# Kernel optimization log

Hardware: AMD Instinct MI355X
Metric: run time of the kernel (lower is better)

## Reference

```python
import jax, jax.numpy as jnp
import numpy as np

N_WIRES = 16
VAR_DEPTH = 2
BATCH = 16


def _param_sizes():
    sizes = []
    n = N_WIRES
    lay = 0
    while n > 1:
        sizes.append(4 * int(np.ceil(N_WIRES / 2 ** lay)) * VAR_DEPTH)
        n = (n + 1) // 2
        lay += 1
    return sizes  # [128, 64, 32, 16]


def _apply_1q(psi, gate, w):
    # psi: (B, 2, ..., 2); gate: (2,2) complex; wire w lives on axis w+1
    psi = jnp.moveaxis(psi, w + 1, -1)
    psi = jnp.einsum('...j,ij->...i', psi, gate)
    return jnp.moveaxis(psi, -1, w + 1)


def _rx(psi, th, w):
    c = jnp.cos(th / 2).astype(jnp.complex64)
    s = jnp.sin(th / 2).astype(jnp.complex64)
    gate = jnp.stack([jnp.stack([c, -1j * s]), jnp.stack([-1j * s, c])])
    return _apply_1q(psi, gate, w)


def _rz(psi, th, w):
    ph = jnp.exp(0.5j * th * jnp.array([-1.0, 1.0], jnp.float32)).astype(jnp.complex64)
    shape = [1] * psi.ndim
    shape[w + 1] = 2
    return psi * ph.reshape(shape)


def _rzz(psi, th, wa, wb):
    # diag(e^{-i t/2}, e^{i t/2}, e^{i t/2}, e^{-i t/2}) -> sign = -1 if bits equal else +1
    sgn = jnp.array([[-1.0, 1.0], [1.0, -1.0]], jnp.float32)
    ph = jnp.exp(0.5j * th * sgn).astype(jnp.complex64)  # symmetric, transpose-safe
    a, b = min(wa, wb) + 1, max(wa, wb) + 1
    shape = [1] * psi.ndim
    shape[a] = 2
    shape[b] = 2
    return psi * ph.reshape(shape)


def _cnot(psi, c, t):
    p0 = jax.lax.slice_in_dim(psi, 0, 1, axis=c + 1)
    p1 = jax.lax.slice_in_dim(psi, 1, 2, axis=c + 1)
    return jnp.concatenate([p0, jnp.flip(p1, axis=t + 1)], axis=c + 1)


def _conv_layer(psi, params, active):
    n = len(active)
    for d in range(VAR_DEPTH):
        for j in range(n):
            base = 4 * j + d * 4 * n
            psi = _rx(psi, params[base + 0], active[j])
            psi = _rz(psi, params[base + 1], active[j])
            psi = _rx(psi, params[base + 2], active[j])
        for bg in (0, 1):
            for j in range(bg, n, 2):
                jn = (j + 1) % n  # ring coupling (wraps last->first)
                base = 4 * j + d * 4 * n
                psi = _rzz(psi, params[base + 3], active[j], active[jn])
    return psi


def _pool(psi, active):
    for j in range(0, len(active), 2):
        if j + 1 < len(active):
            psi = _cnot(psi, active[j], active[j + 1])
    return psi, active[::2]


def _forward(psi, params_list):
    active = list(range(N_WIRES))
    for p in params_list:
        psi = _conv_layer(psi, p, active)
        if len(active) > 1:
            psi, active = _pool(psi, active)
    w = active[0]  # measure Z on the surviving wire (wire 0)
    prob = psi.real ** 2 + psi.imag ** 2
    axes = tuple(a for a in range(1, psi.ndim) if a != w + 1)
    p2 = prob.sum(axis=axes)  # (B, 2)
    return p2[:, 0] - p2[:, 1]


def setup_inputs() -> dict:
    key = jax.random.key(0)
    ks = jax.random.split(key, 8)
    dim = 2 ** N_WIRES
    x_re = jax.random.normal(ks[0], (BATCH, dim), dtype=jnp.float32)
    x_im = jax.random.normal(ks[1], (BATCH, dim), dtype=jnp.float32)
    nrm = jnp.sqrt(jnp.sum(x_re ** 2 + x_im ** 2, axis=1, keepdims=True))
    x_re = x_re / nrm
    x_im = x_im / nrm
    sizes = _param_sizes()
    two_pi = 2.0 * np.pi
    params = [jax.random.uniform(ks[2 + i], (sizes[i],), dtype=jnp.float32) * two_pi
              for i in range(len(sizes))]
    return {"x_re": x_re, "x_im": x_im,
            "params0": params[0], "params1": params[1],
            "params2": params[2], "params3": params[3]}


def reference(x_re, x_im, params0, params1, params2, params3):
    psi = (x_re + 1j * x_im).astype(jnp.complex64)
    psi = psi.reshape((BATCH,) + (2,) * N_WIRES)
    return _forward(psi, [params0, params1, params2, params3])
```

## Files before the change

kernel.cpp:

```cpp
#include <hip/hip_runtime.h>


#define DEV __device__ __forceinline__
#define TB(i) (tbl + (i)*8)

__device__ static const unsigned char G_CP[60] = {
  15,14,13,12,11,10,9,8,7,6,5,4,3,2,1,0,
  15,14,13,12,11,10,9,8,7,6,5,4,3,2,1,0,
  15,13,11,9,7,5,3,1,
  15,13,11,9,7,5,3,1,
  15,11,7,3,
  15,11,7,3,
  15,7,
  15,7
};
__device__ static const unsigned char G_CQ[60] = {
  14,13,12,11,10,9,8,7,6,5,4,3,2,1,0,15,
  14,13,12,11,10,9,8,7,6,5,4,3,2,1,0,15,
  13,11,9,7,5,3,1,15,
  13,11,9,7,5,3,1,15,
  11,7,3,15,
  11,7,3,15,
  7,15,
  7,15
};

DEV float2 F2(float x, float y){ float2 r; r.x = x; r.y = y; return r; }
DEV float2 cmulf(float2 a, float2 b){ return F2(a.x*b.x - a.y*b.y, a.x*b.y + a.y*b.x); }
DEV int swz(int j){ return j ^ ((j>>4)&15) ^ ((j>>6)&15); }

template<int B>
DEV void gate8(float2* a, const float* __restrict__ g){
  float u00r=g[0],u00i=g[1],u01r=g[2],u01i=g[3],u10r=g[4],u10i=g[5],u11r=g[6],u11i=g[7];
  #pragma unroll
  for (int m=0; m<4; m++){
    int i0 = ((m>>B)<<(B+1)) | (m & ((1<<B)-1));
    int i1 = i0 | (1<<B);
    float2 x0=a[i0], x1=a[i1];
    a[i0] = F2(u00r*x0.x - u00i*x0.y + u01r*x1.x - u01i*x1.y,
               u00r*x0.y + u00i*x0.x + u01r*x1.y + u01i*x1.x);
    a[i1] = F2(u10r*x0.x - u10i*x0.y + u11r*x1.x - u11i*x1.y,
               u10r*x0.y + u10i*x0.x + u11r*x1.y + u11i*x1.x);
  }
}

template<int CB,int TB>
DEV void cnot8(float2* a){
  #pragma unroll
  for (int r=0; r<8; r++){
    if ( ((r>>CB)&1)==1 && ((r>>TB)&1)==0 ){
      float2 tmp = a[r]; a[r] = a[r | (1<<TB)]; a[r | (1<<TB)] = tmp;
    }
  }
}

template<int C0,int N,unsigned M0,unsigned M1,unsigned M2>
DEV void diag8(float2* a, const float* __restrict__ tbl, unsigned Ib){
  const unsigned regmask = M0|M1|M2;
  float2 F0 = F2(1.f, 0.f);
  #pragma unroll
  for (int k=0; k<N; k++){
    const int p = G_CP[C0+k], q = G_CQ[C0+k];
    if ( !(((1u<<p)|(1u<<q)) & regmask) ){
      float c = tbl[480 + 2*(C0+k)], s = tbl[481 + 2*(C0+k)];
      unsigned x = ((Ib>>p) ^ (Ib>>q)) & 1u;
      F0 = cmulf(F0, F2(c, x ? s : -s));
    }
  }
  #pragma unroll
  for (int r=0; r<8; r++){
    unsigned Ir = Ib ^ ((r&1)?M0:0u) ^ ((r&2)?M1:0u) ^ ((r&4)?M2:0u);
    float2 ph = F0;
    #pragma unroll
    for (int k=0; k<N; k++){
      const int p = G_CP[C0+k], q = G_CQ[C0+k];
      if ( ((1u<<p)|(1u<<q)) & regmask ){
        float c = tbl[480 + 2*(C0+k)], s = tbl[481 + 2*(C0+k)];
        unsigned x = ((Ir>>p) ^ (Ir>>q)) & 1u;
        ph = cmulf(ph, F2(c, x ? s : -s));
      }
    }
    a[r] = cmulf(a[r], ph);
  }
}

__global__ void k_setup(const float* __restrict__ p0, const float* __restrict__ p1,
                        const float* __restrict__ p2, const float* __restrict__ p3,
                        float* __restrict__ tbl, float* __restrict__ out){
  int g = threadIdx.x;
  if (g < 16) out[g] = 0.f;
  if (g >= 60) return;
  int d, j, n; const float* P;
  if (g < 32)      { n=16; d=(g>>4)&1; j=g&15; P=p0; }
  else if (g < 48) { n=8;  d=(g>>3)&1; j=g&7;  P=p1; }
  else if (g < 56) { n=4;  d=(g>>2)&1; j=g&3;  P=p2; }
  else             { n=2;  d=(g>>1)&1; j=g&1;  P=p3; }
  int base = 4*j + 4*n*d;
  double th0 = P[base+0], th1 = P[base+1], th2 = P[base+2], th3 = P[base+3];
  double c0 = cos(th0*0.5), s0 = sin(th0*0.5);
  double ca = cos(th1*0.5), sa = sin(th1*0.5);
  double c2 = cos(th2*0.5), s2 = sin(th2*0.5);
  double B00r =  ca*c0, B00i = -sa*c0;
  double B01r = -sa*s0, B01i = -ca*s0;
  double B10r =  sa*s0, B10i = -ca*s0;
  double B11r =  ca*c0, B11i =  sa*c0;
  double U00r = c2*B00r + s2*B10i, U00i = c2*B00i - s2*B10r;
  double U01r = c2*B01r + s2*B11i, U01i = c2*B01i - s2*B11r;
  double U10r = s2*B00i + c2*B10r, U10i = -s2*B00r + c2*B10i;
  double U11r = s2*B01i + c2*B11r, U11i = -s2*B01r + c2*B11i;
  float* o = tbl + g*8;
  o[0]=(float)U00r; o[1]=(float)U00i; o[2]=(float)U01r; o[3]=(float)U01i;
  o[4]=(float)U10r; o[5]=(float)U10i; o[6]=(float)U11r; o[7]=(float)U11i;
  tbl[480 + 2*g] = (float)cos(th3*0.5);
  tbl[481 + 2*g] = (float)sin(th3*0.5);
}

__global__ __launch_bounds__(128) void k_pass1(const float* __restrict__ xre, const float* __restrict__ xim,
                                               const float* __restrict__ tbl, float2* __restrict__ st){
  const int t = threadIdx.x;
  const int batch = blockIdx.x >> 6, o = blockIdx.x & 63;
  const unsigned hi = ((unsigned)batch<<16) | ((unsigned)o<<10);
  __shared__ float2 lds[2][1024];
  float2 a[8];
  {
    unsigned base = hi | ((unsigned)t<<3);
    float4 r0 = *(const float4*)(xre+base), r1 = *(const float4*)(xre+base+4);
    float4 i0 = *(const float4*)(xim+base), i1 = *(const float4*)(xim+base+4);
    a[0]=F2(r0.x,i0.x); a[1]=F2(r0.y,i0.y); a[2]=F2(r0.z,i0.z); a[3]=F2(r0.w,i0.w);
    a[4]=F2(r1.x,i1.x); a[5]=F2(r1.y,i1.y); a[6]=F2(r1.z,i1.z); a[7]=F2(r1.w,i1.w);
  }
  gate8<0>(a, TB(15)); gate8<1>(a, TB(14)); gate8<2>(a, TB(13));
  #pragma unroll
  for (int r=0;r<8;r++) lds[0][swz(r | (t<<3))] = a[r];
  __syncthreads();
  #pragma unroll
  for (int r=0;r<8;r++) a[r] = lds[0][swz((t&7) | (r<<3) | ((t>>3)<<6))];
  gate8<0>(a, TB(12)); gate8<1>(a, TB(11)); gate8<2>(a, TB(10));
  #pragma unroll
  for (int r=0;r<8;r++) lds[1][swz((t&7) | (r<<3) | ((t>>3)<<6))] = a[r];
  __syncthreads();
  #pragma unroll
  for (int r=0;r<8;r++) a[r] = lds[1][swz((t&63) | (r<<6) | ((t>>6)<<9))];
  gate8<0>(a, TB(9)); gate8<1>(a, TB(8)); gate8<2>(a, TB(7));
  #pragma unroll
  for (int r=0;r<8;r++) lds[0][swz((t&63) | (r<<6) | ((t>>6)<<9))] = a[r];
  __syncthreads();
  #pragma unroll
  for (int r=0;r<8;r++) a[r] = lds[0][swz(t | (r<<7))];
  gate8<2>(a, TB(6));
  #pragma unroll
  for (int r=0;r<8;r++) st[hi | (unsigned)(t | (r<<7))] = a[r];
}

DEV unsigned p2I(int j, int o){ return (unsigned)((j&15) | (o<<4) | ((j>>4)<<10)); }

__global__ __launch_bounds__(128) void k_pass2(const float* __restrict__ tbl, float2* __restrict__ st){
  const int t = threadIdx.x;
  const int batch = blockIdx.x >> 6, o = blockIdx.x & 63;
  const unsigned bb = (unsigned)batch<<16;
  __shared__ float2 lds[2][1024];
  float2 a[8];
  #pragma unroll
  for (int r=0;r<8;r++) a[r] = st[bb | p2I(t | (r<<7), o)];
  gate8<0>(a, TB(2)); gate8<1>(a, TB(1)); gate8<2>(a, TB(0));
  #pragma unroll
  for (int r=0;r<8;r++) lds[0][swz(t | (r<<7))] = a[r];
  __syncthreads();
  #pragma unroll
  for (int r=0;r<8;r++) a[r] = lds[0][swz((t&15) | (r<<4) | ((t>>4)<<7))];
  gate8<0>(a, TB(5)); gate8<1>(a, TB(4)); gate8<2>(a, TB(3));
  diag8<0,16, (1u<<10),(1u<<11),(1u<<12)>(a, tbl, p2I((t&15) | ((t>>4)<<7), o));
  gate8<0>(a, TB(21)); gate8<1>(a, TB(20)); gate8<2>(a, TB(19));
  #pragma unroll
  for (int r=0;r<8;r++) lds[1][swz((t&15) | (r<<4) | ((t>>4)<<7))] = a[r];
  __syncthreads();
  #pragma unroll
  for (int r=0;r<8;r++) a[r] = lds[1][swz(t | (r<<7))];
  gate8<0>(a, TB(18)); gate8<1>(a, TB(17)); gate8<2>(a, TB(16));
  #pragma unroll
  for (int r=0;r<8;r++) lds[0][swz(t | (r<<7))] = a[r];
  __syncthreads();
  #pragma unroll
  for (int r=0;r<8;r++) a[r] = lds[0][swz(r | (t<<3))];
  gate8<0>(a, TB(31)); gate8<1>(a, TB(30)); gate8<2>(a, TB(29));
  #pragma unroll
  for (int r=0;r<8;r++) lds[1][swz(r | (t<<3))] = a[r];
  __syncthreads();
  #pragma unroll
  for (int r=0;r<8;r++) a[r] = lds[1][swz((t&7) | (r<<3) | ((t>>3)<<6))];
  gate8<0>(a, TB(28));
  #pragma unroll
  for (int r=0;r<8;r++) st[bb | p2I((t&7) | (r<<3) | ((t>>3)<<6), o)] = a[r];
}

__global__ __launch_bounds__(128) void k_pass3(const float* __restrict__ tbl, float2* __restrict__ st){
  const int t = threadIdx.x;
  const int batch = blockIdx.x >> 6, o = blockIdx.x & 63;
  const unsigned hi = ((unsigned)batch<<16) | ((unsigned)o<<10);
  __shared__ float2 lds[2][1024];
  float2 a[8];
  #pragma unroll
  for (int r=0;r<8;r++) a[r] = st[hi | (unsigned)((t&15) | (r<<4) | ((t>>4)<<7))];
  gate8<0>(a, TB(27)); gate8<1>(a, TB(26)); gate8<2>(a, TB(25));
  #pragma unroll
  for (int r=0;r<8;r++) lds[0][swz((t&15) | (r<<4) | ((t>>4)<<7))] = a[r];
  __syncthreads();
  #pragma unroll
  for (int r=0;r<8;r++) a[r] = lds[0][swz(t | (r<<7))];
  gate8<0>(a, TB(24)); gate8<1>(a, TB(23)); gate8<2>(a, TB(22));
  diag8<16,16, (1u<<7),(1u<<8),(1u<<9)>(a, tbl, (unsigned)t | ((unsigned)o<<10));
  #pragma unroll
  for (int r=0;r<8;r++) st[hi | (unsigned)(t | (r<<7))] = a[r];
}

DEV unsigned p4I(int j, unsigned og){
  return (unsigned)( (j&15) | (((j>>4)&1)<<5) | (((j>>5)&1)<<7) | (((j>>6)&1)<<9)
                   | (((j>>7)&1)<<11) | (((j>>8)&1)<<13) | (((j>>9)&1)<<15) ) | og;
}
DEV int p4_jA(int t,int r){ return t | (r<<7); }
DEV int p4_jB(int t,int r){ return (t&15) | (r<<4) | ((t>>4)<<7); }
DEV int p4_jC(int t,int r){ return (t&1) | ((r&1)<<1) | (((t>>1)&1)<<2) | (((r>>1)&1)<<3)
                                  | (((t>>2)&1)<<4) | (((r>>2)&1)<<5) | ((t>>3)<<6); }
DEV int p4_jD(int t,int r){ return (t&15) | ((r&1)<<4) | (((t>>4)&1)<<5) | (((r>>1)&1)<<6)
                                  | (((t>>5)&1)<<7) | (((r>>2)&1)<<8) | ((t>>6)<<9); }
DEV int p4_jF(int t,int r){ return (t&63) | ((r&1)<<6) | (((r>>1)&1)<<7) | (((t>>6)&1)<<8) | ((r>>2)<<9); }
DEV int p4_jG(int t,int r){ return (t&15) | ((r&3)<<4) | (((t>>4)&7)<<6) | ((r>>2)<<9); }
DEV int p4_jJ(int t,int r){ return (t&7) | ((r&1)<<3) | (((t>>3)&1)<<4) | (((r>>1)&1)<<5)
                                  | (((t>>4)&7)<<6) | ((r>>2)<<9); }

__global__ __launch_bounds__(128) void k_pass4(const float* __restrict__ tbl, float2* __restrict__ st,
                                               float* __restrict__ out){
  const int t = threadIdx.x;
  const int batch = blockIdx.x >> 6, o = blockIdx.x & 63;
  const unsigned bb = (unsigned)batch<<16;
  const unsigned og = ((unsigned)(o&1)<<4) | ((unsigned)(o&2)<<5) | ((unsigned)(o&4)<<6)
                    | ((unsigned)(o&8)<<7) | ((unsigned)(o&16)<<8) | ((unsigned)(o&32)<<9);
  __shared__ float2 lds[2][1024];
  float2 a[8];
  #pragma unroll
  for (int r=0;r<8;r++){
    unsigned I = p4I(p4_jA(t,r), og);
    unsigned s1 = I ^ ((I & 0xAAAAu) >> 1);
    a[r] = st[bb | s1];
  }
  gate8<0>(a, TB(34)); gate8<1>(a, TB(33)); gate8<2>(a, TB(32));
  #pragma unroll
  for (int r=0;r<8;r++) lds[0][swz(p4_jA(t,r))] = a[r];
  __syncthreads();
  #pragma unroll
  for (int r=0;r<8;r++) a[r] = lds[0][swz(p4_jB(t,r))];
  gate8<0>(a, TB(37)); gate8<1>(a, TB(36)); gate8<2>(a, TB(35));
  #pragma unroll
  for (int r=0;r<8;r++) lds[1][swz(p4_jB(t,r))] = a[r];
  __syncthreads();
  #pragma unroll
  for (int r=0;r<8;r++) a[r] = lds[1][swz(p4_jC(t,r))];
  gate8<0>(a, TB(39)); gate8<1>(a, TB(38));
  diag8<32,8, 2u,8u,128u>(a, tbl, p4I(p4_jC(t,0), og));
  gate8<0>(a, TB(47)); gate8<1>(a, TB(46)); gate8<2>(a, TB(44));
  #pragma unroll
  for (int r=0;r<8;r++) lds[0][swz(p4_jC(t,r))] = a[r];
  __syncthreads();
  #pragma unroll
  for (int r=0;r<8;r++) a[r] = lds[0][swz(p4_jD(t,r))];
  gate8<0>(a, TB(45)); gate8<1>(a, TB(43)); gate8<2>(a, TB(41));
  #pragma unroll
  for (int r=0;r<8;r++) lds[1][swz(p4_jD(t,r))] = a[r];
  __syncthreads();
  #pragma unroll
  for (int r=0;r<8;r++) a[r] = lds[1][swz(p4_jA(t,r))];
  gate8<0>(a, TB(42)); gate8<2>(a, TB(40));
  diag8<40,8, (1u<<11),(1u<<13),(1u<<15)>(a, tbl, p4I(p4_jA(t,0), og));
  cnot8<2,1>(a);
  gate8<2>(a, TB(48));
  #pragma unroll
  for (int r=0;r<8;r++) lds[0][swz(p4_jA(t,r))] = a[r];
  __syncthreads();
  #pragma unroll
  for (int r=0;r<8;r++) a[r] = lds[0][swz(p4_jF(t,r))];
  cnot8<1,0>(a);
  gate8<1>(a, TB(49));
  #pragma unroll
  for (int r=0;r<8;r++) lds[1][swz(p4_jF(t,r))] = a[r];
  __syncthreads();
  #pragma unroll
  for (int r=0;r<8;r++) a[r] = lds[1][swz(p4_jG(t,r))];
  cnot8<1,0>(a);
  gate8<1>(a, TB(50));
  #pragma unroll
  for (int r=0;r<8;r++) lds[0][swz(p4_jG(t,r))] = a[r];
  __syncthreads();
  #pragma unroll
  for (int r=0;r<8;r++) a[r] = lds[0][swz(p4_jC(t,r))];
  cnot8<1,0>(a);
  gate8<1>(a, TB(51));
  diag8<48,4, 2u,8u,128u>(a, tbl, p4I(p4_jC(t,0), og));
  gate8<1>(a, TB(55)); gate8<2>(a, TB(54));
  #pragma unroll
  for (int r=0;r<8;r++) lds[1][swz(p4_jC(t,r))] = a[r];
  __syncthreads();
  #pragma unroll
  for (int r=0;r<8;r++) a[r] = lds[1][swz(p4_jA(t,r))];
  gate8<0>(a, TB(53)); gate8<2>(a, TB(52));
  diag8<52,4, (1u<<11),(1u<<13),(1u<<15)>(a, tbl, p4I(p4_jA(t,0), og));
  cnot8<2,0>(a);
  gate8<2>(a, TB(56));
  #pragma unroll
  for (int r=0;r<8;r++) lds[0][swz(p4_jA(t,r))] = a[r];
  __syncthreads();
  #pragma unroll
  for (int r=0;r<8;r++) a[r] = lds[0][swz(p4_jJ(t,r))];
  cnot8<1,0>(a);
  gate8<1>(a, TB(57));
  diag8<56,2, 8u,128u,(1u<<15)>(a, tbl, p4I(p4_jJ(t,0), og));
  gate8<2>(a, TB(58));
  float s = 0.f;
  #pragma unroll
  for (int r=0;r<8;r++){
    float w = a[r].x*a[r].x + a[r].y*a[r].y;
    s += (r & 4) ? -w : w;
  }
  #pragma unroll
  for (int off=32; off>0; off>>=1) s += __shfl_down(s, off);
  __syncthreads();
  float* red = reinterpret_cast<float*>(lds);
  if ((t & 63) == 0) red[t>>6] = s;
  __syncthreads();
  if (t == 0) atomicAdd(out + batch, red[0] + red[1]);
}

extern "C" void kernel_launch(void* const* d_in, const int* in_sizes, int n_in,
                              void* d_out, int out_size, void* d_ws, size_t ws_size,
                              hipStream_t stream) {
  const float* xre = (const float*)d_in[0];
  const float* xim = (const float*)d_in[1];
  const float* p0  = (const float*)d_in[2];
  const float* p1  = (const float*)d_in[3];
  const float* p2  = (const float*)d_in[4];
  const float* p3  = (const float*)d_in[5];
  float* out = (float*)d_out;
  float* tbl = (float*)d_ws;
  float2* st = (float2*)((char*)d_ws + 16384);

  k_setup<<<1, 64, 0, stream>>>(p0, p1, p2, p3, tbl, out);
  k_pass1<<<1024, 128, 0, stream>>>(xre, xim, tbl, st);
  k_pass2<<<1024, 128, 0, stream>>>(tbl, st);
  k_pass3<<<1024, 128, 0, stream>>>(tbl, st);
  k_pass4<<<1024, 128, 0, stream>>>(tbl, st, out);
}
```

Measured before the change: 122.8 us.

## Fuse setup and four passes into one persistent kernel with grid barriers

```diff
diff --git a/kernel.cpp b/kernel.cpp
--- a/kernel.cpp
+++ b/kernel.cpp
@@ -2,7 +2,9 @@
 
 
 #define DEV __device__ __forceinline__
-#define TB(i) (tbl + (i)*8)
+#define TB(i) (tbs + (i)*8)
+
+#define NBLK 512u
 
 __device__ static const unsigned char G_CP[60] = {
   15,14,13,12,11,10,9,8,7,6,5,4,3,2,1,0,
@@ -29,8 +31,21 @@
 DEV float2 cmulf(float2 a, float2 b){ return F2(a.x*b.x - a.y*b.y, a.x*b.y + a.y*b.x); }
 DEV int swz(int j){ return j ^ ((j>>4)&15) ^ ((j>>6)&15); }
 
+DEV void gbar(unsigned* cnt){
+  __syncthreads();
+  if (threadIdx.x == 0){
+    __threadfence();
+    __hip_atomic_fetch_add(cnt, 1u, __ATOMIC_ACQ_REL, __HIP_MEMORY_SCOPE_AGENT);
+    while (__hip_atomic_load(cnt, __ATOMIC_ACQUIRE, __HIP_MEMORY_SCOPE_AGENT) < NBLK){
+      __builtin_amdgcn_s_sleep(2);
+    }
+  }
+  __syncthreads();
+  __threadfence();
+}
+
 template<int B>
-DEV void gate8(float2* a, const float* __restrict__ g){
+DEV void gate8(float2* a, const float* g){
   float u00r=g[0],u00i=g[1],u01r=g[2],u01i=g[3],u10r=g[4],u10i=g[5],u11r=g[6],u11i=g[7];
   #pragma unroll
   for (int m=0; m<4; m++){
@@ -44,25 +59,25 @@
   }
 }
 
-template<int CB,int TB>
+template<int CB,int TBIT>
 DEV void cnot8(float2* a){
   #pragma unroll
   for (int r=0; r<8; r++){
-    if ( ((r>>CB)&1)==1 && ((r>>TB)&1)==0 ){
-      float2 tmp = a[r]; a[r] = a[r | (1<<TB)]; a[r | (1<<TB)] = tmp;
+    if ( ((r>>CB)&1)==1 && ((r>>TBIT)&1)==0 ){
+      float2 tmp = a[r]; a[r] = a[r | (1<<TBIT)]; a[r | (1<<TBIT)] = tmp;
     }
   }
 }
 
 template<int C0,int N,unsigned M0,unsigned M1,unsigned M2>
-DEV void diag8(float2* a, const float* __restrict__ tbl, unsigned Ib){
+DEV void diag8(float2* a, const float* tbs, unsigned Ib){
   const unsigned regmask = M0|M1|M2;
   float2 F0 = F2(1.f, 0.f);
   #pragma unroll
   for (int k=0; k<N; k++){
     const int p = G_CP[C0+k], q = G_CQ[C0+k];
     if ( !(((1u<<p)|(1u<<q)) & regmask) ){
-      float c = tbl[480 + 2*(C0+k)], s = tbl[481 + 2*(C0+k)];
+      float c = tbs[480 + 2*(C0+k)], s = tbs[481 + 2*(C0+k)];
       unsigned x = ((Ib>>p) ^ (Ib>>q)) & 1u;
       F0 = cmulf(F0, F2(c, x ? s : -s));
     }
@@ -75,7 +90,7 @@
     for (int k=0; k<N; k++){
       const int p = G_CP[C0+k], q = G_CQ[C0+k];
       if ( ((1u<<p)|(1u<<q)) & regmask ){
-        float c = tbl[480 + 2*(C0+k)], s = tbl[481 + 2*(C0+k)];
+        float c = tbs[480 + 2*(C0+k)], s = tbs[481 + 2*(C0+k)];
         unsigned x = ((Ir>>p) ^ (Ir>>q)) & 1u;
         ph = cmulf(ph, F2(c, x ? s : -s));
       }
@@ -84,135 +99,7 @@
   }
 }
 
-__global__ void k_setup(const float* __restrict__ p0, const float* __restrict__ p1,
-                        const float* __restrict__ p2, const float* __restrict__ p3,
-                        float* __restrict__ tbl, float* __restrict__ out){
-  int g = threadIdx.x;
-  if (g < 16) out[g] = 0.f;
-  if (g >= 60) return;
-  int d, j, n; const float* P;
-  if (g < 32)      { n=16; d=(g>>4)&1; j=g&15; P=p0; }
-  else if (g < 48) { n=8;  d=(g>>3)&1; j=g&7;  P=p1; }
-  else if (g < 56) { n=4;  d=(g>>2)&1; j=g&3;  P=p2; }
-  else             { n=2;  d=(g>>1)&1; j=g&1;  P=p3; }
-  int base = 4*j + 4*n*d;
-  double th0 = P[base+0], th1 = P[base+1], th2 = P[base+2], th3 = P[base+3];
-  double c0 = cos(th0*0.5), s0 = sin(th0*0.5);
-  double ca = cos(th1*0.5), sa = sin(th1*0.5);
-  double c2 = cos(th2*0.5), s2 = sin(th2*0.5);
-  double B00r =  ca*c0, B00i = -sa*c0;
-  double B01r = -sa*s0, B01i = -ca*s0;
-  double B10r =  sa*s0, B10i = -ca*s0;
-  double B11r =  ca*c0, B11i =  sa*c0;
-  double U00r = c2*B00r + s2*B10i, U00i = c2*B00i - s2*B10r;
-  double U01r = c2*B01r + s2*B11i, U01i = c2*B01i - s2*B11r;
-  double U10r = s2*B00i + c2*B10r, U10i = -s2*B00r + c2*B10i;
-  double U11r = s2*B01i + c2*B11r, U11i = -s2*B01r + c2*B11i;
-  float* o = tbl + g*8;
-  o[0]=(float)U00r; o[1]=(float)U00i; o[2]=(float)U01r; o[3]=(float)U01i;
-  o[4]=(float)U10r; o[5]=(float)U10i; o[6]=(float)U11r; o[7]=(float)U11i;
-  tbl[480 + 2*g] = (float)cos(th3*0.5);
-  tbl[481 + 2*g] = (float)sin(th3*0.5);
-}
-
-__global__ __launch_bounds__(128) void k_pass1(const float* __restrict__ xre, const float* __restrict__ xim,
-                                               const float* __restrict__ tbl, float2* __restrict__ st){
-  const int t = threadIdx.x;
-  const int batch = blockIdx.x >> 6, o = blockIdx.x & 63;
-  const unsigned hi = ((unsigned)batch<<16) | ((unsigned)o<<10);
-  __shared__ float2 lds[2][1024];
-  float2 a[8];
-  {
-    unsigned base = hi | ((unsigned)t<<3);
-    float4 r0 = *(const float4*)(xre+base), r1 = *(const float4*)(xre+base+4);
-    float4 i0 = *(const float4*)(xim+base), i1 = *(const float4*)(xim+base+4);
-    a[0]=F2(r0.x,i0.x); a[1]=F2(r0.y,i0.y); a[2]=F2(r0.z,i0.z); a[3]=F2(r0.w,i0.w);
-    a[4]=F2(r1.x,i1.x); a[5]=F2(r1.y,i1.y); a[6]=F2(r1.z,i1.z); a[7]=F2(r1.w,i1.w);
-  }
-  gate8<0>(a, TB(15)); gate8<1>(a, TB(14)); gate8<2>(a, TB(13));
-  #pragma unroll
-  for (int r=0;r<8;r++) lds[0][swz(r | (t<<3))] = a[r];
-  __syncthreads();
-  #pragma unroll
-  for (int r=0;r<8;r++) a[r] = lds[0][swz((t&7) | (r<<3) | ((t>>3)<<6))];
-  gate8<0>(a, TB(12)); gate8<1>(a, TB(11)); gate8<2>(a, TB(10));
-  #pragma unroll
-  for (int r=0;r<8;r++) lds[1][swz((t&7) | (r<<3) | ((t>>3)<<6))] = a[r];
-  __syncthreads();
-  #pragma unroll
-  for (int r=0;r<8;r++) a[r] = lds[1][swz((t&63) | (r<<6) | ((t>>6)<<9))];
-  gate8<0>(a, TB(9)); gate8<1>(a, TB(8)); gate8<2>(a, TB(7));
-  #pragma unroll
-  for (int r=0;r<8;r++) lds[0][swz((t&63) | (r<<6) | ((t>>6)<<9))] = a[r];
-  __syncthreads();
-  #pragma unroll
-  for (int r=0;r<8;r++) a[r] = lds[0][swz(t | (r<<7))];
-  gate8<2>(a, TB(6));
-  #pragma unroll
-  for (int r=0;r<8;r++) st[hi | (unsigned)(t | (r<<7))] = a[r];
-}
-
 DEV unsigned p2I(int j, int o){ return (unsigned)((j&15) | (o<<4) | ((j>>4)<<10)); }
-
-__global__ __launch_bounds__(128) void k_pass2(const float* __restrict__ tbl, float2* __restrict__ st){
-  const int t = threadIdx.x;
-  const int batch = blockIdx.x >> 6, o = blockIdx.x & 63;
-  const unsigned bb = (unsigned)batch<<16;
-  __shared__ float2 lds[2][1024];
-  float2 a[8];
-  #pragma unroll
-  for (int r=0;r<8;r++) a[r] = st[bb | p2I(t | (r<<7), o)];
-  gate8<0>(a, TB(2)); gate8<1>(a, TB(1)); gate8<2>(a, TB(0));
-  #pragma unroll
-  for (int r=0;r<8;r++) lds[0][swz(t | (r<<7))] = a[r];
-  __syncthreads();
-  #pragma unroll
-  for (int r=0;r<8;r++) a[r] = lds[0][swz((t&15) | (r<<4) | ((t>>4)<<7))];
-  gate8<0>(a, TB(5)); gate8<1>(a, TB(4)); gate8<2>(a, TB(3));
-  diag8<0,16, (1u<<10),(1u<<11),(1u<<12)>(a, tbl, p2I((t&15) | ((t>>4)<<7), o));
-  gate8<0>(a, TB(21)); gate8<1>(a, TB(20)); gate8<2>(a, TB(19));
-  #pragma unroll
-  for (int r=0;r<8;r++) lds[1][swz((t&15) | (r<<4) | ((t>>4)<<7))] = a[r];
-  __syncthreads();
-  #pragma unroll
-  for (int r=0;r<8;r++) a[r] = lds[1][swz(t | (r<<7))];
-  gate8<0>(a, TB(18)); gate8<1>(a, TB(17)); gate8<2>(a, TB(16));
-  #pragma unroll
-  for (int r=0;r<8;r++) lds[0][swz(t | (r<<7))] = a[r];
-  __syncthreads();
-  #pragma unroll
-  for (int r=0;r<8;r++) a[r] = lds[0][swz(r | (t<<3))];
-  gate8<0>(a, TB(31)); gate8<1>(a, TB(30)); gate8<2>(a, TB(29));
-  #pragma unroll
-  for (int r=0;r<8;r++) lds[1][swz(r | (t<<3))] = a[r];
-  __syncthreads();
-  #pragma unroll
-  for (int r=0;r<8;r++) a[r] = lds[1][swz((t&7) | (r<<3) | ((t>>3)<<6))];
-  gate8<0>(a, TB(28));
-  #pragma unroll
-  for (int r=0;r<8;r++) st[bb | p2I((t&7) | (r<<3) | ((t>>3)<<6), o)] = a[r];
-}
-
-__global__ __launch_bounds__(128) void k_pass3(const float* __restrict__ tbl, float2* __restrict__ st){
-  const int t = threadIdx.x;
-  const int batch = blockIdx.x >> 6, o = blockIdx.x & 63;
-  const unsigned hi = ((unsigned)batch<<16) | ((unsigned)o<<10);
-  __shared__ float2 lds[2][1024];
-  float2 a[8];
-  #pragma unroll
-  for (int r=0;r<8;r++) a[r] = st[hi | (unsigned)((t&15) | (r<<4) | ((t>>4)<<7))];
-  gate8<0>(a, TB(27)); gate8<1>(a, TB(26)); gate8<2>(a, TB(25));
-  #pragma unroll
-  for (int r=0;r<8;r++) lds[0][swz((t&15) | (r<<4) | ((t>>4)<<7))] = a[r];
-  __syncthreads();
-  #pragma unroll
-  for (int r=0;r<8;r++) a[r] = lds[0][swz(t | (r<<7))];
-  gate8<0>(a, TB(24)); gate8<1>(a, TB(23)); gate8<2>(a, TB(22));
-  diag8<16,16, (1u<<7),(1u<<8),(1u<<9)>(a, tbl, (unsigned)t | ((unsigned)o<<10));
-  #pragma unroll
-  for (int r=0;r<8;r++) st[hi | (unsigned)(t | (r<<7))] = a[r];
-}
-
 DEV unsigned p4I(int j, unsigned og){
   return (unsigned)( (j&15) | (((j>>4)&1)<<5) | (((j>>5)&1)<<7) | (((j>>6)&1)<<9)
                    | (((j>>7)&1)<<11) | (((j>>8)&1)<<13) | (((j>>9)&1)<<15) ) | og;
@@ -228,91 +115,222 @@
 DEV int p4_jJ(int t,int r){ return (t&7) | ((r&1)<<3) | (((t>>3)&1)<<4) | (((r>>1)&1)<<5)
                                   | (((t>>4)&7)<<6) | ((r>>2)<<9); }
 
-__global__ __launch_bounds__(128) void k_pass4(const float* __restrict__ tbl, float2* __restrict__ st,
-                                               float* __restrict__ out){
-  const int t = threadIdx.x;
-  const int batch = blockIdx.x >> 6, o = blockIdx.x & 63;
+__global__ __launch_bounds__(256, 2)
+void k_fused(const float* __restrict__ xre, const float* __restrict__ xim,
+             const float* __restrict__ p0, const float* __restrict__ p1,
+             const float* __restrict__ p2, const float* __restrict__ p3,
+             float2* __restrict__ st, unsigned* __restrict__ bar,
+             float* __restrict__ out){
+  const int t  = threadIdx.x;
+  const int ti = t & 127;
+  const int half = t >> 7;
+  const int tile = (blockIdx.x << 1) | half;
+  const int batch = tile >> 6, o = tile & 63;
   const unsigned bb = (unsigned)batch<<16;
+  const unsigned hi10 = bb | ((unsigned)o<<10);
+  __shared__ float2 lds[2048];
+  __shared__ float tbs[600];
+  __shared__ float red[4];
+  float2* L = lds + (half<<10);
+  float2 a[8];
+
+  if (t < 60){
+    int g = t;
+    int d, j, n; const float* P;
+    if (g < 32)      { n=16; d=(g>>4)&1; j=g&15; P=p0; }
+    else if (g < 48) { n=8;  d=(g>>3)&1; j=g&7;  P=p1; }
+    else if (g < 56) { n=4;  d=(g>>2)&1; j=g&3;  P=p2; }
+    else             { n=2;  d=(g>>1)&1; j=g&1;  P=p3; }
+    int base = 4*j + 4*n*d;
+    double th0 = P[base+0], th1 = P[base+1], th2 = P[base+2], th3 = P[base+3];
+    double c0 = cos(th0*0.5), s0 = sin(th0*0.5);
+    double ca = cos(th1*0.5), sa = sin(th1*0.5);
+    double c2 = cos(th2*0.5), s2 = sin(th2*0.5);
+    double B00r =  ca*c0, B00i = -sa*c0;
+    double B01r = -sa*s0, B01i = -ca*s0;
+    double B10r =  sa*s0, B10i = -ca*s0;
+    double B11r =  ca*c0, B11i =  sa*c0;
+    float* oo = tbs + g*8;
+    oo[0]=(float)(c2*B00r + s2*B10i); oo[1]=(float)(c2*B00i - s2*B10r);
+    oo[2]=(float)(c2*B01r + s2*B11i); oo[3]=(float)(c2*B01i - s2*B11r);
+    oo[4]=(float)(s2*B00i + c2*B10r); oo[5]=(float)(-s2*B00r + c2*B10i);
+    oo[6]=(float)(s2*B01i + c2*B11r); oo[7]=(float)(-s2*B01r + c2*B11i);
+    tbs[480 + 2*g] = (float)cos(th3*0.5);
+    tbs[481 + 2*g] = (float)sin(th3*0.5);
+  }
+  __syncthreads();
+
+  {
+    unsigned base = hi10 | ((unsigned)ti<<3);
+    float4 r0 = *(const float4*)(xre+base), r1 = *(const float4*)(xre+base+4);
+    float4 i0 = *(const float4*)(xim+base), i1 = *(const float4*)(xim+base+4);
+    a[0]=F2(r0.x,i0.x); a[1]=F2(r0.y,i0.y); a[2]=F2(r0.z,i0.z); a[3]=F2(r0.w,i0.w);
+    a[4]=F2(r1.x,i1.x); a[5]=F2(r1.y,i1.y); a[6]=F2(r1.z,i1.z); a[7]=F2(r1.w,i1.w);
+  }
+  gate8<0>(a, TB(15)); gate8<1>(a, TB(14)); gate8<2>(a, TB(13));
+  #pragma unroll
+  for (int r=0;r<8;r++) L[swz(r | (ti<<3))] = a[r];
+  __syncthreads();
+  #pragma unroll
+  for (int r=0;r<8;r++) a[r] = L[swz((ti&7) | (r<<3) | ((ti>>3)<<6))];
+  __syncthreads();
+  gate8<0>(a, TB(12)); gate8<1>(a, TB(11)); gate8<2>(a, TB(10));
+  #pragma unroll
+  for (int r=0;r<8;r++) L[swz((ti&7) | (r<<3) | ((ti>>3)<<6))] = a[r];
+  __syncthreads();
+  #pragma unroll
+  for (int r=0;r<8;r++) a[r] = L[swz((ti&63) | (r<<6) | ((ti>>6)<<9))];
+  __syncthreads();
+  gate8<0>(a, TB(9)); gate8<1>(a, TB(8)); gate8<2>(a, TB(7));
+  #pragma unroll
+  for (int r=0;r<8;r++) L[swz((ti&63) | (r<<6) | ((ti>>6)<<9))] = a[r];
+  __syncthreads();
+  #pragma unroll
+  for (int r=0;r<8;r++) a[r] = L[swz(ti | (r<<7))];
+  gate8<2>(a, TB(6));
+  #pragma unroll
+  for (int r=0;r<8;r++) st[hi10 | (unsigned)(ti | (r<<7))] = a[r];
+
+  gbar(bar+0);
+
+  #pragma unroll
+  for (int r=0;r<8;r++) a[r] = st[bb | p2I(ti | (r<<7), o)];
+  gate8<0>(a, TB(2)); gate8<1>(a, TB(1)); gate8<2>(a, TB(0));
+  #pragma unroll
+  for (int r=0;r<8;r++) L[swz(ti | (r<<7))] = a[r];
+  __syncthreads();
+  #pragma unroll
+  for (int r=0;r<8;r++) a[r] = L[swz((ti&15) | (r<<4) | ((ti>>4)<<7))];
+  __syncthreads();
+  gate8<0>(a, TB(5)); gate8<1>(a, TB(4)); gate8<2>(a, TB(3));
+  diag8<0,16, (1u<<10),(1u<<11),(1u<<12)>(a, tbs, p2I((ti&15) | ((ti>>4)<<7), o));
+  gate8<0>(a, TB(21)); gate8<1>(a, TB(20)); gate8<2>(a, TB(19));
+  #pragma unroll
+  for (int r=0;r<8;r++) L[swz((ti&15) | (r<<4) | ((ti>>4)<<7))] = a[r];
+  __syncthreads();
+  #pragma unroll
+  for (int r=0;r<8;r++) a[r] = L[swz(ti | (r<<7))];
+  __syncthreads();
+  gate8<0>(a, TB(18)); gate8<1>(a, TB(17)); gate8<2>(a, TB(16));
+  #pragma unroll
+  for (int r=0;r<8;r++) L[swz(ti | (r<<7))] = a[r];
+  __syncthreads();
+  #pragma unroll
+  for (int r=0;r<8;r++) a[r] = L[swz(r | (ti<<3))];
+  __syncthreads();
+  gate8<0>(a, TB(31)); gate8<1>(a, TB(30)); gate8<2>(a, TB(29));
+  #pragma unroll
+  for (int r=0;r<8;r++) L[swz(r | (ti<<3))] = a[r];
+  __syncthreads();
+  #pragma unroll
+  for (int r=0;r<8;r++) a[r] = L[swz((ti&7) | (r<<3) | ((ti>>3)<<6))];
+  gate8<0>(a, TB(28));
+  #pragma unroll
+  for (int r=0;r<8;r++) st[bb | p2I((ti&7) | (r<<3) | ((ti>>3)<<6), o)] = a[r];
+
+  gbar(bar+1);
+
+  #pragma unroll
+  for (int r=0;r<8;r++) a[r] = st[hi10 | (unsigned)((ti&15) | (r<<4) | ((ti>>4)<<7))];
+  gate8<0>(a, TB(27)); gate8<1>(a, TB(26)); gate8<2>(a, TB(25));
+  #pragma unroll
+  for (int r=0;r<8;r++) L[swz((ti&15) | (r<<4) | ((ti>>4)<<7))] = a[r];
+  __syncthreads();
+  #pragma unroll
+  for (int r=0;r<8;r++) a[r] = L[swz(ti | (r<<7))];
+  gate8<0>(a, TB(24)); gate8<1>(a, TB(23)); gate8<2>(a, TB(22));
+  diag8<16,16, (1u<<7),(1u<<8),(1u<<9)>(a, tbs, (unsigned)ti | ((unsigned)o<<10));
+  #pragma unroll
+  for (int r=0;r<8;r++) st[hi10 | (unsigned)(ti | (r<<7))] = a[r];
+
+  gbar(bar+2);
+
   const unsigned og = ((unsigned)(o&1)<<4) | ((unsigned)(o&2)<<5) | ((unsigned)(o&4)<<6)
                     | ((unsigned)(o&8)<<7) | ((unsigned)(o&16)<<8) | ((unsigned)(o&32)<<9);
-  __shared__ float2 lds[2][1024];
-  float2 a[8];
   #pragma unroll
   for (int r=0;r<8;r++){
-    unsigned I = p4I(p4_jA(t,r), og);
+    unsigned I = p4I(p4_jA(ti,r), og);
     unsigned s1 = I ^ ((I & 0xAAAAu) >> 1);
     a[r] = st[bb | s1];
   }
   gate8<0>(a, TB(34)); gate8<1>(a, TB(33)); gate8<2>(a, TB(32));
   #pragma unroll
-  for (int r=0;r<8;r++) lds[0][swz(p4_jA(t,r))] = a[r];
-  __syncthreads();
-  #pragma unroll
-  for (int r=0;r<8;r++) a[r] = lds[0][swz(p4_jB(t,r))];
+  for (int r=0;r<8;r++) L[swz(p4_jA(ti,r))] = a[r];
+  __syncthreads();
+  #pragma unroll
+  for (int r=0;r<8;r++) a[r] = L[swz(p4_jB(ti,r))];
+  __syncthreads();
   gate8<0>(a, TB(37)); gate8<1>(a, TB(36)); gate8<2>(a, TB(35));
   #pragma unroll
-  for (int r=0;r<8;r++) lds[1][swz(p4_jB(t,r))] = a[r];
-  __syncthreads();
-  #pragma unroll
-  for (int r=0;r<8;r++) a[r] = lds[1][swz(p4_jC(t,r))];
+  for (int r=0;r<8;r++) L[swz(p4_jB(ti,r))] = a[r];
+  __syncthreads();
+  #pragma unroll
+  for (int r=0;r<8;r++) a[r] = L[swz(p4_jC(ti,r))];
+  __syncthreads();
   gate8<0>(a, TB(39)); gate8<1>(a, TB(38));
-  diag8<32,8, 2u,8u,128u>(a, tbl, p4I(p4_jC(t,0), og));
+  diag8<32,8, 2u,8u,128u>(a, tbs, p4I(p4_jC(ti,0), og));
   gate8<0>(a, TB(47)); gate8<1>(a, TB(46)); gate8<2>(a, TB(44));
   #pragma unroll
-  for (int r=0;r<8;r++) lds[0][swz(p4_jC(t,r))] = a[r];
-  __syncthreads();
-  #pragma unroll
-  for (int r=0;r<8;r++) a[r] = lds[0][swz(p4_jD(t,r))];
+  for (int r=0;r<8;r++) L[swz(p4_jC(ti,r))] = a[r];
+  __syncthreads();
+  #pragma unroll
+  for (int r=0;r<8;r++) a[r] = L[swz(p4_jD(ti,r))];
+  __syncthreads();
   gate8<0>(a, TB(45)); gate8<1>(a, TB(43)); gate8<2>(a, TB(41));
   #pragma unroll
-  for (int r=0;r<8;r++) lds[1][swz(p4_jD(t,r))] = a[r];
-  __syncthreads();
-  #pragma unroll
-  for (int r=0;r<8;r++) a[r] = lds[1][swz(p4_jA(t,r))];
+  for (int r=0;r<8;r++) L[swz(p4_jD(ti,r))] = a[r];
+  __syncthreads();
+  #pragma unroll
+  for (int r=0;r<8;r++) a[r] = L[swz(p4_jA(ti,r))];
+  __syncthreads();
   gate8<0>(a, TB(42)); gate8<2>(a, TB(40));
-  diag8<40,8, (1u<<11),(1u<<13),(1u<<15)>(a, tbl, p4I(p4_jA(t,0), og));
+  diag8<40,8, (1u<<11),(1u<<13),(1u<<15)>(a, tbs, p4I(p4_jA(ti,0), og));
   cnot8<2,1>(a);
   gate8<2>(a, TB(48));
   #pragma unroll
-  for (int r=0;r<8;r++) lds[0][swz(p4_jA(t,r))] = a[r];
-  __syncthreads();
-  #pragma unroll
-  for (int r=0;r<8;r++) a[r] = lds[0][swz(p4_jF(t,r))];
+  for (int r=0;r<8;r++) L[swz(p4_jA(ti,r))] = a[r];
+  __syncthreads();
+  #pragma unroll
+  for (int r=0;r<8;r++) a[r] = L[swz(p4_jF(ti,r))];
+  __syncthreads();
   cnot8<1,0>(a);
   gate8<1>(a, TB(49));
   #pragma unroll
-  for (int r=0;r<8;r++) lds[1][swz(p4_jF(t,r))] = a[r];
-  __syncthreads();
-  #pragma unroll
-  for (int r=0;r<8;r++) a[r] = lds[1][swz(p4_jG(t,r))];
+  for (int r=0;r<8;r++) L[swz(p4_jF(ti,r))] = a[r];
+  __syncthreads();
+  #pragma unroll
+  for (int r=0;r<8;r++) a[r] = L[swz(p4_jG(ti,r))];
+  __syncthreads();
   cnot8<1,0>(a);
   gate8<1>(a, TB(50));
   #pragma unroll
-  for (int r=0;r<8;r++) lds[0][swz(p4_jG(t,r))] = a[r];
-  __syncthreads();
-  #pragma unroll
-  for (int r=0;r<8;r++) a[r] = lds[0][swz(p4_jC(t,r))];
+  for (int r=0;r<8;r++) L[swz(p4_jG(ti,r))] = a[r];
+  __syncthreads();
+  #pragma unroll
+  for (int r=0;r<8;r++) a[r] = L[swz(p4_jC(ti,r))];
+  __syncthreads();
   cnot8<1,0>(a);
   gate8<1>(a, TB(51));
-  diag8<48,4, 2u,8u,128u>(a, tbl, p4I(p4_jC(t,0), og));
+  diag8<48,4, 2u,8u,128u>(a, tbs, p4I(p4_jC(ti,0), og));
   gate8<1>(a, TB(55)); gate8<2>(a, TB(54));
   #pragma unroll
-  for (int r=0;r<8;r++) lds[1][swz(p4_jC(t,r))] = a[r];
-  __syncthreads();
-  #pragma unroll
-  for (int r=0;r<8;r++) a[r] = lds[1][swz(p4_jA(t,r))];
+  for (int r=0;r<8;r++) L[swz(p4_jC(ti,r))] = a[r];
+  __syncthreads();
+  #pragma unroll
+  for (int r=0;r<8;r++) a[r] = L[swz(p4_jA(ti,r))];
+  __syncthreads();
   gate8<0>(a, TB(53)); gate8<2>(a, TB(52));
-  diag8<52,4, (1u<<11),(1u<<13),(1u<<15)>(a, tbl, p4I(p4_jA(t,0), og));
+  diag8<52,4, (1u<<11),(1u<<13),(1u<<15)>(a, tbs, p4I(p4_jA(ti,0), og));
   cnot8<2,0>(a);
   gate8<2>(a, TB(56));
   #pragma unroll
-  for (int r=0;r<8;r++) lds[0][swz(p4_jA(t,r))] = a[r];
-  __syncthreads();
-  #pragma unroll
-  for (int r=0;r<8;r++) a[r] = lds[0][swz(p4_jJ(t,r))];
+  for (int r=0;r<8;r++) L[swz(p4_jA(ti,r))] = a[r];
+  __syncthreads();
+  #pragma unroll
+  for (int r=0;r<8;r++) a[r] = L[swz(p4_jJ(ti,r))];
   cnot8<1,0>(a);
   gate8<1>(a, TB(57));
-  diag8<56,2, 8u,128u,(1u<<15)>(a, tbl, p4I(p4_jJ(t,0), og));
+  diag8<56,2, 8u,128u,(1u<<15)>(a, tbs, p4I(p4_jJ(ti,0), og));
   gate8<2>(a, TB(58));
   float s = 0.f;
   #pragma unroll
@@ -322,11 +340,9 @@
   }
   #pragma unroll
   for (int off=32; off>0; off>>=1) s += __shfl_down(s, off);
-  __syncthreads();
-  float* red = reinterpret_cast<float*>(lds);
   if ((t & 63) == 0) red[t>>6] = s;
   __syncthreads();
-  if (t == 0) atomicAdd(out + batch, red[0] + red[1]);
+  if (ti == 0) atomicAdd(out + batch, red[(t>>6)] + red[(t>>6)+1]);
 }
 
 extern "C" void kernel_launch(void* const* d_in, const int* in_sizes, int n_in,
@@ -339,12 +355,10 @@
   const float* p2  = (const float*)d_in[4];
   const float* p3  = (const float*)d_in[5];
   float* out = (float*)d_out;
-  float* tbl = (float*)d_ws;
-  float2* st = (float2*)((char*)d_ws + 16384);
-
-  k_setup<<<1, 64, 0, stream>>>(p0, p1, p2, p3, tbl, out);
-  k_pass1<<<1024, 128, 0, stream>>>(xre, xim, tbl, st);
-  k_pass2<<<1024, 128, 0, stream>>>(tbl, st);
-  k_pass3<<<1024, 128, 0, stream>>>(tbl, st);
-  k_pass4<<<1024, 128, 0, stream>>>(tbl, st, out);
-}
+  float2* st = (float2*)d_ws;
+  unsigned* bar = (unsigned*)((char*)d_ws + (8u<<20));
+
+  hipMemsetAsync(bar, 0, 3*sizeof(unsigned), stream);
+  hipMemsetAsync(out, 0, 16*sizeof(float), stream);
+  k_fused<<<dim3(NBLK), dim3(256), 0, stream>>>(xre, xim, p0, p1, p2, p3, st, bar, out);
+}
```

Measured after the change: 331.7 us. 2.7x slower.
